# Performance work log

Measured on AMD Instinct MI355X. Metric: run time of the kernel, lower is better.

The kernel has to match this reference:

```python
import jax, jax.numpy as jnp
import numpy as np

COS_EPS = 1e-08


def setup_inputs() -> dict:
    key = jax.random.key(0)
    k1, k2, k3, k4, k5 = jax.random.split(key, 5)
    B, N, C = 4, 4096, 128
    q_node = jax.random.normal(k1, (B, N, C), dtype=jnp.float32)
    k_node = jax.random.normal(k2, (B, N, C), dtype=jnp.float32)
    v_node = jax.random.normal(k3, (B, N, C), dtype=jnp.float32)
    # shared Linear(h_dim, h_dim): torch default init scale ~ 1/sqrt(C)
    W = jax.random.normal(k4, (C, C), dtype=jnp.float32) / jnp.sqrt(jnp.float32(C))
    b = jax.random.normal(k5, (C,), dtype=jnp.float32) / jnp.sqrt(jnp.float32(C))
    return {"q_node": q_node, "k_node": k_node, "v_node": v_node, "W": W, "b": b}


def reference(q_node, k_node, v_node, W, b):
    # shared projection applied to q, k, v
    q = jnp.einsum('bnc,cd->bnd', q_node, W.T) + b
    k = jnp.einsum('bnc,cd->bnd', k_node, W.T) + b
    v = jnp.einsum('bnc,cd->bnd', v_node, W.T) + b
    # cosine similarity scores: [B, Nq, Nk]
    qn = jnp.linalg.norm(q, axis=2, keepdims=True)        # [B, Nq, 1]
    kn = jnp.linalg.norm(k, axis=2, keepdims=True)        # [B, Nk, 1]
    scores = jnp.einsum('bqc,bkc->bqk', q, k)
    cos_sim = scores / (qn * jnp.swapaxes(kn, 1, 2) + COS_EPS)
    # sum-normalization (not softmax)
    edge_weight = cos_sim / (cos_sim.sum(axis=2, keepdims=True) + 1e-08)
    # weighted aggregation: [B, Nq, C]
    return jnp.einsum('bqk,bkc->bqc', edge_weight, v)
```

## Files before the change

kernel.cpp:

```cpp
#include <hip/hip_runtime.h>

#define BB 4
#define NN 4096
#define CC 128
#define NROWS (BB * NN)

#define QN_OFF  0
#define QP_OFF  (QN_OFF + NROWS)
#define MM_OFF  (QP_OFF + NROWS * CC)
#define KS_OFF  (MM_OFF + BB * CC * CC)
#define PP_OFF  (KS_OFF + BB * CC)
#define KP_OFF  (PP_OFF + 256 * CC * CC)

__device__ __forceinline__ void fma4(float4& a, const float4 x,
    const float4 w0, const float4 w1, const float4 w2, const float4 w3)
{
    a.x += x.x * w0.x + x.y * w1.x + x.z * w2.x + x.w * w3.x;
    a.y += x.x * w0.y + x.y * w1.y + x.z * w2.y + x.w * w3.y;
    a.z += x.x * w0.z + x.y * w1.z + x.z * w2.z + x.w * w3.z;
    a.w += x.x * w0.w + x.y * w1.w + x.z * w2.w + x.w * w3.w;
}

__device__ __forceinline__ float dot4(const float4 x, const float4 k)
{
    return x.x * k.x + x.y * k.y + x.z * k.z + x.w * k.w;
}

__global__ __launch_bounds__(512, 2) void projpb_kernel(
    const float* __restrict__ q_node, const float* __restrict__ k_node,
    const float* __restrict__ v_node, const float* __restrict__ W,
    const float* __restrict__ bias, float* __restrict__ ws)
{
    __shared__ float S[CC * CC];
    __shared__ float4 red[512];
    const int tid = threadIdx.x;

    for (int e = tid; e < CC * CC; e += 512) {
        int d = e >> 7, c = e & 127;
        S[(c << 7) + ((((d >> 2) ^ (c & 31)) << 2) | (d & 3))] = W[e];
    }

    const int blk  = blockIdx.x;
    const int base = blk * 64;
    const int dg = tid & 31;
    const int rg = tid >> 5;

    float4 bias4 = ((const float4*)bias)[dg];
    float4 acc[8];
#pragma unroll
    for (int i = 0; i < 8; i++) acc[i] = bias4;

    __syncthreads();

    const float4* Qv = (const float4*)(q_node + (size_t)(base + rg * 4) * CC);
    const float4* Kv = (const float4*)(k_node + (size_t)(base + rg * 4) * CC);
    const float4* Sv = (const float4*)S;

#define LW(s0, s1, s2, s3, c)                              \
    s0 = Sv[(((c) + 0) << 5) + (dg ^ (((c) + 0) & 31))];   \
    s1 = Sv[(((c) + 1) << 5) + (dg ^ (((c) + 1) & 31))];   \
    s2 = Sv[(((c) + 2) << 5) + (dg ^ (((c) + 2) & 31))];   \
    s3 = Sv[(((c) + 3) << 5) + (dg ^ (((c) + 3) & 31))];
#define LX(xq, xk, c)                                      \
    { const int c4_ = (c) >> 2;                            \
      xq[0] = Qv[c4_];      xq[1] = Qv[32 + c4_];          \
      xq[2] = Qv[64 + c4_]; xq[3] = Qv[96 + c4_];          \
      xk[0] = Kv[c4_];      xk[1] = Kv[32 + c4_];          \
      xk[2] = Kv[64 + c4_]; xk[3] = Kv[96 + c4_]; }
#define FM(w0, w1, w2, w3, xq, xk)                         \
    fma4(acc[0], xq[0], w0, w1, w2, w3);                   \
    fma4(acc[1], xq[1], w0, w1, w2, w3);                   \
    fma4(acc[2], xq[2], w0, w1, w2, w3);                   \
    fma4(acc[3], xq[3], w0, w1, w2, w3);                   \
    fma4(acc[4], xk[0], w0, w1, w2, w3);                   \
    fma4(acc[5], xk[1], w0, w1, w2, w3);                   \
    fma4(acc[6], xk[2], w0, w1, w2, w3);                   \
    fma4(acc[7], xk[3], w0, w1, w2, w3);

    {
        float4 wA0, wA1, wA2, wA3, wB0, wB1, wB2, wB3;
        float4 xqA[4], xkA[4], xqB[4], xkB[4];

        LW(wA0, wA1, wA2, wA3, 0)
        LX(xqA, xkA, 0)
        for (int c = 0; c <= CC - 16; c += 8) {
            LW(wB0, wB1, wB2, wB3, c + 4)
            LX(xqB, xkB, c + 4)
            FM(wA0, wA1, wA2, wA3, xqA, xkA)
            LW(wA0, wA1, wA2, wA3, c + 8)
            LX(xqA, xkA, c + 8)
            FM(wB0, wB1, wB2, wB3, xqB, xkB)
        }
        LW(wB0, wB1, wB2, wB3, CC - 4)
        LX(xqB, xkB, CC - 4)
        FM(wA0, wA1, wA2, wA3, xqA, xkA)
        FM(wB0, wB1, wB2, wB3, xqB, xkB)
    }
#undef LW
#undef LX
#undef FM

#pragma unroll
    for (int i = 0; i < 4; i++) {
        const int rq = base + rg * 4 + i;
        float ss = acc[i].x * acc[i].x + acc[i].y * acc[i].y
                 + acc[i].z * acc[i].z + acc[i].w * acc[i].w;
#pragma unroll
        for (int off = 16; off > 0; off >>= 1) ss += __shfl_xor(ss, off, 32);
        ((float4*)(ws + QP_OFF + (size_t)rq * CC))[dg] = acc[i];
        if (dg == 0) ws[QN_OFF + rq] = sqrtf(ss);
    }

    __syncthreads();

    float* Khs = S;
    float* Vs  = S + 8192;

#pragma unroll
    for (int i = 0; i < 4; i++) {
        float ss = acc[4 + i].x * acc[4 + i].x + acc[4 + i].y * acc[4 + i].y
                 + acc[4 + i].z * acc[4 + i].z + acc[4 + i].w * acc[4 + i].w;
#pragma unroll
        for (int off = 16; off > 0; off >>= 1) ss += __shfl_xor(ss, off, 32);
        float inv = 1.0f / sqrtf(ss);
        float4 o = acc[4 + i];
        o.x *= inv; o.y *= inv; o.z *= inv; o.w *= inv;
        ((float4*)(Khs + (rg * 4 + i) * CC))[dg] = o;
    }

    const int c4v = tid & 31, nrv = tid >> 5;
    const float* Vp = v_node + (size_t)base * CC;
#pragma unroll
    for (int i = 0; i < 4; i++) {
        int n = nrv + i * 16;
        ((float4*)(Vs + n * CC))[c4v] = ((const float4*)(Vp + (size_t)n * CC))[c4v];
    }
    __syncthreads();

    float4 ksum4 = make_float4(0.f, 0.f, 0.f, 0.f);
#pragma unroll
    for (int i = 0; i < 4; i++) {
        int n = nrv + i * 16;
        float4 kv = ((const float4*)(Khs + n * CC))[c4v];
        ksum4.x += kv.x; ksum4.y += kv.y; ksum4.z += kv.z; ksum4.w += kv.w;
    }

    const int dg2 = tid & 15, cg = tid >> 4;
    float a2[4][8];
#pragma unroll
    for (int i = 0; i < 4; i++)
#pragma unroll
        for (int j = 0; j < 8; j++) a2[i][j] = 0.f;

#define P2L(ka, va, vb, n)                                  \
    ka = *(const float4*)(Khs + (n) * CC + 4 * cg);         \
    va = *(const float4*)(Vs + (n) * CC + 4 * dg2);         \
    vb = *(const float4*)(Vs + (n) * CC + 64 + 4 * dg2);
#define P2F(ka, va, vb)                                     \
    {  float kc[4] = {ka.x, ka.y, ka.z, ka.w};              \
       float vd[8] = {va.x, va.y, va.z, va.w,               \
                      vb.x, vb.y, vb.z, vb.w};              \
       _Pragma("unroll")                                    \
       for (int i = 0; i < 4; i++)                          \
           { _Pragma("unroll")                              \
             for (int j = 0; j < 8; j++)                    \
                 a2[i][j] += kc[i] * vd[j]; } }

    {
        float4 kaA, vaA, vbA, kaB, vaB, vbB;
        P2L(kaA, vaA, vbA, 0)
        for (int n = 0; n <= 60; n += 2) {
            P2L(kaB, vaB, vbB, n + 1)
            P2F(kaA, vaA, vbA)
            P2L(kaA, vaA, vbA, n + 2)
            P2F(kaB, vaB, vbB)
        }
        P2L(kaB, vaB, vbB, 63)
        P2F(kaA, vaA, vbA)
        P2F(kaB, vaB, vbB)
    }
#undef P2L
#undef P2F

    float* pp = ws + PP_OFF + (size_t)blk * (CC * CC);
#pragma unroll
    for (int i = 0; i < 4; i++) {
        int c = 4 * cg + i;
        *(float4*)(pp + c * CC + 4 * dg2) =
            make_float4(a2[i][0], a2[i][1], a2[i][2], a2[i][3]);
        *(float4*)(pp + c * CC + 64 + 4 * dg2) =
            make_float4(a2[i][4], a2[i][5], a2[i][6], a2[i][7]);
    }

    red[nrv * 32 + c4v] = ksum4;
    __syncthreads();
    if (tid < 32) {
        float4 sm = red[tid];
#pragma unroll
        for (int i = 1; i < 16; i++) {
            float4 t = red[i * 32 + tid];
            sm.x += t.x; sm.y += t.y; sm.z += t.z; sm.w += t.w;
        }
        ((float4*)(ws + KP_OFF + (size_t)blk * CC))[tid] = sm;
    }
}

__global__ __launch_bounds__(256) void mchain_kernel(const float* __restrict__ W,
                                                     const float* __restrict__ bias,
                                                     float* __restrict__ ws)
{
    __shared__ float4 W4s[CC * 32];
    __shared__ float4 m0q[4][2][32];
    __shared__ float m0row[2][CC];
    __shared__ float kpart[4];
    __shared__ float ksl[2];
    const int tid = threadIdx.x;
    const int b = blockIdx.y, x = blockIdx.x;
    const int c0 = x * 2;

    for (int idx = tid; idx < CC * 32; idx += 256) {
        int e = idx >> 5, d4 = idx & 31;
        W4s[(e << 5) + (d4 ^ (e & 31))] = ((const float4*)W)[idx];
    }

    {
        const int q  = tid >> 6;
        const int r  = (tid >> 5) & 1;
        const int c4 = tid & 31;
        const float4* pp = (const float4*)(ws + PP_OFF
                         + (size_t)(b * 64 + q * 16) * (CC * CC)
                         + (size_t)(c0 + r) * CC) + c4;
        float4 s0 = make_float4(0.f, 0.f, 0.f, 0.f);
#pragma unroll 4
        for (int p = 0; p < 16; p++) {
            float4 t = pp[(size_t)p * (CC * CC / 4)];
            s0.x += t.x; s0.y += t.y; s0.z += t.z; s0.w += t.w;
        }
        m0q[q][r][c4] = s0;
    }

    {
        const int rr = tid >> 7, p = tid & 127;
        float v = 0.f;
        if (p < 64) v = ws[KP_OFF + (size_t)(b * 64 + p) * CC + c0 + rr];
#pragma unroll
        for (int off = 32; off > 0; off >>= 1) v += __shfl_xor(v, off, 64);
        if ((tid & 63) == 0) kpart[tid >> 6] = v;
    }
    __syncthreads();

    if (tid < 64) {
        const int r = tid >> 5, c4 = tid & 31;
        float4 a = m0q[0][r][c4], bq = m0q[1][r][c4];
        float4 c = m0q[2][r][c4], d = m0q[3][r][c4];
        float4 s;
        s.x = (a.x + bq.x) + (c.x + d.x);
        s.y = (a.y + bq.y) + (c.y + d.y);
        s.z = (a.z + bq.z) + (c.z + d.z);
        s.w = (a.w + bq.w) + (c.w + d.w);
        ((float4*)&m0row[r][0])[c4] = s;
    }
    if (tid < 2) {
        float s = kpart[tid * 2] + kpart[tid * 2 + 1];
        ksl[tid] = s;
        ws[KS_OFF + b * CC + c0 + tid] = s;
    }
    __syncthreads();

    const int r = tid >> 7, e = tid & 127;
    const float4* mr = (const float4*)m0row[r];
    float m = 0.f;
#pragma unroll
    for (int d4 = 0; d4 < 32; d4++) {
        float4 a4 = mr[d4];
        float4 w4 = W4s[(e << 5) + (d4 ^ (e & 31))];
        m += a4.x * w4.x + a4.y * w4.y + a4.z * w4.z + a4.w * w4.w;
    }
    m += ksl[r] * bias[e];
    ws[MM_OFF + (size_t)b * CC * CC + (size_t)(c0 + r) * CC + e] = m;
}

__global__ __launch_bounds__(512, 2) void out_kernel(const float* __restrict__ ws,
                                                     float* __restrict__ out)
{
    __shared__ float Ml[CC * CC];

    const int blk = blockIdx.x;
    const int b = blk >> 6;
    const int r0 = (blk & 63) * 64;
    const float* M = ws + MM_OFF + (size_t)b * CC * CC;
    const int tid = threadIdx.x;

    for (int e = tid; e < CC * CC / 4; e += 512)
        ((float4*)Ml)[e] = ((const float4*)M)[e];

    const float4* Ks4 = (const float4*)(ws + KS_OFF + b * CC);
    const int dg = tid & 31, rg = tid >> 5;
    const int row = r0 + rg * 4;
    const float4* Qv = (const float4*)(ws + QP_OFF + ((size_t)b * NN + row) * CC);
    const float4* Mv = (const float4*)Ml;

    float4 acc[4];
    float s[4];
#pragma unroll
    for (int i = 0; i < 4; i++) {
        acc[i] = make_float4(0.f, 0.f, 0.f, 0.f);
        s[i] = 0.f;
    }

    __syncthreads();

#define OLW(m0, m1, m2, m3, ks, c)               \
    m0 = Mv[(((c) + 0) << 5) + dg];              \
    m1 = Mv[(((c) + 1) << 5) + dg];              \
    m2 = Mv[(((c) + 2) << 5) + dg];              \
    m3 = Mv[(((c) + 3) << 5) + dg];              \
    ks = Ks4[(c) >> 2];
#define OLX(xv, c)                                 \
    { const int c4_ = (c) >> 2;                    \
      xv[0] = Qv[c4_];      xv[1] = Qv[32 + c4_];  \
      xv[2] = Qv[64 + c4_]; xv[3] = Qv[96 + c4_]; }
#define OFM(m0, m1, m2, m3, ks, xv)                  \
    _Pragma("unroll")                                \
    for (int i_ = 0; i_ < 4; i_++) {                 \
        fma4(acc[i_], xv[i_], m0, m1, m2, m3);       \
        s[i_] += dot4(xv[i_], ks);                   \
    }

    {
        float4 mA0, mA1, mA2, mA3, mB0, mB1, mB2, mB3;
        float4 ksA, ksB, xA[4], xB[4];
        OLW(mA0, mA1, mA2, mA3, ksA, 0)
        OLX(xA, 0)
        for (int c = 0; c <= CC - 16; c += 8) {
            OLW(mB0, mB1, mB2, mB3, ksB, c + 4)
            OLX(xB, c + 4)
            OFM(mA0, mA1, mA2, mA3, ksA, xA)
            OLW(mA0, mA1, mA2, mA3, ksA, c + 8)
            OLX(xA, c + 8)
            OFM(mB0, mB1, mB2, mB3, ksB, xB)
        }
        OLW(mB0, mB1, mB2, mB3, ksB, CC - 4)
        OLX(xB, CC - 4)
        OFM(mA0, mA1, mA2, mA3, ksA, xA)
        OFM(mB0, mB1, mB2, mB3, ksB, xB)
    }
#undef OLW
#undef OLX
#undef OFM

    float* op = out + ((size_t)b * NN + row) * CC;
    const float* qn = ws + QN_OFF + (size_t)b * NN + row;
#pragma unroll
    for (int i = 0; i < 4; i++) {
        float inv = 1.0f / (s[i] + 1e-8f * qn[i]);
        float4 o = acc[i];
        o.x *= inv; o.y *= inv; o.z *= inv; o.w *= inv;
        ((float4*)(op + (size_t)i * CC))[dg] = o;
    }
}

extern "C" void kernel_launch(void* const* d_in, const int* in_sizes, int n_in,
                              void* d_out, int out_size, void* d_ws, size_t ws_size,
                              hipStream_t stream)
{
    const float* q_node = (const float*)d_in[0];
    const float* k_node = (const float*)d_in[1];
    const float* v_node = (const float*)d_in[2];
    const float* W      = (const float*)d_in[3];
    const float* bias   = (const float*)d_in[4];
    float* out = (float*)d_out;
    float* ws  = (float*)d_ws;

    projpb_kernel<<<256, 512, 0, stream>>>(q_node, k_node, v_node, W, bias, ws);
    mchain_kernel<<<dim3(64, BB), 256, 0, stream>>>(W, bias, ws);
    out_kernel<<<256, 512, 0, stream>>>(ws, out);
}
```

Baseline: 131.6 us.

## Use bf16x3 split MFMA for shared Q/K projection in first kernel

Measured after the change: 121.3 us. 1.09x faster.

```diff
diff --git a/kernel.cpp b/kernel.cpp
--- a/kernel.cpp
+++ b/kernel.cpp
@@ -12,6 +12,9 @@
 #define PP_OFF  (KS_OFF + BB * CC)
 #define KP_OFF  (PP_OFF + 256 * CC * CC)
 
+typedef __attribute__((ext_vector_type(8))) short short8;
+typedef __attribute__((ext_vector_type(4))) float f32x4;
+
 __device__ __forceinline__ void fma4(float4& a, const float4 x,
     const float4 w0, const float4 w1, const float4 w2, const float4 w3)
 {
@@ -26,106 +29,132 @@
     return x.x * k.x + x.y * k.y + x.z * k.z + x.w * k.w;
 }
 
-__global__ __launch_bounds__(512, 2) void projpb_kernel(
+__device__ __forceinline__ unsigned short f2bf(float f)
+{
+    union { float f; unsigned u; } v; v.f = f;
+    unsigned r = (v.u + 0x7fffu + ((v.u >> 16) & 1u)) >> 16;
+    return (unsigned short)r;
+}
+__device__ __forceinline__ float bf2f(unsigned short h)
+{
+    union { unsigned u; float f; } v; v.u = ((unsigned)h) << 16;
+    return v.f;
+}
+
+__global__ __launch_bounds__(512, 1) void projpb_kernel(
     const float* __restrict__ q_node, const float* __restrict__ k_node,
     const float* __restrict__ v_node, const float* __restrict__ W,
     const float* __restrict__ bias, float* __restrict__ ws)
 {
-    __shared__ float S[CC * CC];
+    __shared__ __align__(16) unsigned short Wsp[3 * CC * CC];
     __shared__ float4 red[512];
+    unsigned short* Whi = Wsp;
+    unsigned short* Wmd = Wsp + CC * CC;
+    unsigned short* Wlo = Wsp + 2 * CC * CC;
+
     const int tid = threadIdx.x;
 
     for (int e = tid; e < CC * CC; e += 512) {
-        int d = e >> 7, c = e & 127;
-        S[(c << 7) + ((((d >> 2) ^ (c & 31)) << 2) | (d & 3))] = W[e];
+        int col = e >> 7, k = e & 127;
+        float wv = W[e];
+        unsigned short hi = f2bf(wv);
+        float r1 = wv - bf2f(hi);
+        unsigned short md = f2bf(r1);
+        unsigned short lo = f2bf(r1 - bf2f(md));
+        int idx = (col << 7) + ((((k >> 3) ^ (col & 7)) << 3) | (k & 7));
+        Whi[idx] = hi; Wmd[idx] = md; Wlo[idx] = lo;
     }
 
     const int blk  = blockIdx.x;
     const int base = blk * 64;
-    const int dg = tid & 31;
-    const int rg = tid >> 5;
-
-    float4 bias4 = ((const float4*)bias)[dg];
-    float4 acc[8];
-#pragma unroll
-    for (int i = 0; i < 8; i++) acc[i] = bias4;
-
-    __syncthreads();
-
-    const float4* Qv = (const float4*)(q_node + (size_t)(base + rg * 4) * CC);
-    const float4* Kv = (const float4*)(k_node + (size_t)(base + rg * 4) * CC);
-    const float4* Sv = (const float4*)S;
-
-#define LW(s0, s1, s2, s3, c)                              \
-    s0 = Sv[(((c) + 0) << 5) + (dg ^ (((c) + 0) & 31))];   \
-    s1 = Sv[(((c) + 1) << 5) + (dg ^ (((c) + 1) & 31))];   \
-    s2 = Sv[(((c) + 2) << 5) + (dg ^ (((c) + 2) & 31))];   \
-    s3 = Sv[(((c) + 3) << 5) + (dg ^ (((c) + 3) & 31))];
-#define LX(xq, xk, c)                                      \
-    { const int c4_ = (c) >> 2;                            \
-      xq[0] = Qv[c4_];      xq[1] = Qv[32 + c4_];          \
-      xq[2] = Qv[64 + c4_]; xq[3] = Qv[96 + c4_];          \
-      xk[0] = Kv[c4_];      xk[1] = Kv[32 + c4_];          \
-      xk[2] = Kv[64 + c4_]; xk[3] = Kv[96 + c4_]; }
-#define FM(w0, w1, w2, w3, xq, xk)                         \
-    fma4(acc[0], xq[0], w0, w1, w2, w3);                   \
-    fma4(acc[1], xq[1], w0, w1, w2, w3);                   \
-    fma4(acc[2], xq[2], w0, w1, w2, w3);                   \
-    fma4(acc[3], xq[3], w0, w1, w2, w3);                   \
-    fma4(acc[4], xk[0], w0, w1, w2, w3);                   \
-    fma4(acc[5], xk[1], w0, w1, w2, w3);                   \
-    fma4(acc[6], xk[2], w0, w1, w2, w3);                   \
-    fma4(acc[7], xk[3], w0, w1, w2, w3);
-
-    {
-        float4 wA0, wA1, wA2, wA3, wB0, wB1, wB2, wB3;
-        float4 xqA[4], xkA[4], xqB[4], xkB[4];
-
-        LW(wA0, wA1, wA2, wA3, 0)
-        LX(xqA, xkA, 0)
-        for (int c = 0; c <= CC - 16; c += 8) {
-            LW(wB0, wB1, wB2, wB3, c + 4)
-            LX(xqB, xkB, c + 4)
-            FM(wA0, wA1, wA2, wA3, xqA, xkA)
-            LW(wA0, wA1, wA2, wA3, c + 8)
-            LX(xqA, xkA, c + 8)
-            FM(wB0, wB1, wB2, wB3, xqB, xkB)
-        }
-        LW(wB0, wB1, wB2, wB3, CC - 4)
-        LX(xqB, xkB, CC - 4)
-        FM(wA0, wA1, wA2, wA3, xqA, xkA)
-        FM(wB0, wB1, wB2, wB3, xqB, xkB)
-    }
-#undef LW
-#undef LX
-#undef FM
-
-#pragma unroll
-    for (int i = 0; i < 4; i++) {
-        const int rq = base + rg * 4 + i;
-        float ss = acc[i].x * acc[i].x + acc[i].y * acc[i].y
-                 + acc[i].z * acc[i].z + acc[i].w * acc[i].w;
-#pragma unroll
-        for (int off = 16; off > 0; off >>= 1) ss += __shfl_xor(ss, off, 32);
-        ((float4*)(ws + QP_OFF + (size_t)rq * CC))[dg] = acc[i];
-        if (dg == 0) ws[QN_OFF + rq] = sqrtf(ss);
-    }
-
-    __syncthreads();
-
-    float* Khs = S;
-    float* Vs  = S + 8192;
-
-#pragma unroll
-    for (int i = 0; i < 4; i++) {
-        float ss = acc[4 + i].x * acc[4 + i].x + acc[4 + i].y * acc[4 + i].y
-                 + acc[4 + i].z * acc[4 + i].z + acc[4 + i].w * acc[4 + i].w;
-#pragma unroll
-        for (int off = 16; off > 0; off >>= 1) ss += __shfl_xor(ss, off, 32);
-        float inv = 1.0f / sqrtf(ss);
-        float4 o = acc[4 + i];
-        o.x *= inv; o.y *= inv; o.z *= inv; o.w *= inv;
-        ((float4*)(Khs + (rg * 4 + i) * CC))[dg] = o;
+    const int w    = tid >> 6;
+    const int lane = tid & 63;
+    const int l15  = lane & 15;
+    const int lg   = lane >> 4;
+    const bool isq = (w < 4);
+    const int rt   = w & 3;
+    const float* X = isq ? q_node : k_node;
+    const int arow = base + rt * 16 + l15;
+
+    f32x4 acc[8];
+#pragma unroll
+    for (int ct = 0; ct < 8; ct++) {
+        float b = bias[ct * 16 + l15];
+        acc[ct] = (f32x4){b, b, b, b};
+    }
+
+    __syncthreads();
+
+    const float* Xr = X + (size_t)arow * CC;
+#pragma unroll
+    for (int ks = 0; ks < 4; ks++) {
+        const int k0 = ks * 32 + lg * 8;
+        float4 xa = *(const float4*)(Xr + k0);
+        float4 xb = *(const float4*)(Xr + k0 + 4);
+        float xs[8] = {xa.x, xa.y, xa.z, xa.w, xb.x, xb.y, xb.z, xb.w};
+        short8 Ahi, Amd, Alo;
+#pragma unroll
+        for (int j = 0; j < 8; j++) {
+            unsigned short h = f2bf(xs[j]);
+            float r1 = xs[j] - bf2f(h);
+            unsigned short m = f2bf(r1);
+            Ahi[j] = (short)h;
+            Amd[j] = (short)m;
+            Alo[j] = (short)f2bf(r1 - bf2f(m));
+        }
+        const int slot = ks * 4 + lg;
+#pragma unroll
+        for (int ct = 0; ct < 8; ct++) {
+            int col  = ct * 16 + l15;
+            int fidx = (col << 7) + ((slot ^ (col & 7)) << 3);
+            short8 Bhi = *(const short8*)(Whi + fidx);
+            short8 Bmd = *(const short8*)(Wmd + fidx);
+            short8 Blo = *(const short8*)(Wlo + fidx);
+            acc[ct] = __builtin_amdgcn_mfma_f32_16x16x32_bf16(Ahi, Bhi, acc[ct], 0, 0, 0);
+            acc[ct] = __builtin_amdgcn_mfma_f32_16x16x32_bf16(Ahi, Bmd, acc[ct], 0, 0, 0);
+            acc[ct] = __builtin_amdgcn_mfma_f32_16x16x32_bf16(Amd, Bhi, acc[ct], 0, 0, 0);
+            acc[ct] = __builtin_amdgcn_mfma_f32_16x16x32_bf16(Ahi, Blo, acc[ct], 0, 0, 0);
+            acc[ct] = __builtin_amdgcn_mfma_f32_16x16x32_bf16(Amd, Bmd, acc[ct], 0, 0, 0);
+            acc[ct] = __builtin_amdgcn_mfma_f32_16x16x32_bf16(Alo, Bhi, acc[ct], 0, 0, 0);
+        }
+    }
+
+    float ss[4];
+#pragma unroll
+    for (int r = 0; r < 4; r++) {
+        float t = 0.f;
+#pragma unroll
+        for (int ct = 0; ct < 8; ct++) t += acc[ct][r] * acc[ct][r];
+#pragma unroll
+        for (int off = 8; off > 0; off >>= 1) t += __shfl_xor(t, off, 16);
+        ss[r] = t;
+    }
+
+    if (isq) {
+#pragma unroll
+        for (int r = 0; r < 4; r++) {
+            int gr = base + rt * 16 + lg * 4 + r;
+            float* qp = ws + QP_OFF + (size_t)gr * CC;
+#pragma unroll
+            for (int ct = 0; ct < 8; ct++) qp[ct * 16 + l15] = acc[ct][r];
+            if (l15 == 0) ws[QN_OFF + gr] = sqrtf(ss[r]);
+        }
+    }
+
+    __syncthreads();
+
+    float* Khs = (float*)Wsp;
+    float* Vs  = Khs + 8192;
+
+    if (!isq) {
+#pragma unroll
+        for (int r = 0; r < 4; r++) {
+            float inv = 1.0f / sqrtf(ss[r]);
+            int lr = rt * 16 + lg * 4 + r;
+            float* kp = Khs + lr * CC;
+#pragma unroll
+            for (int ct = 0; ct < 8; ct++) kp[ct * 16 + l15] = acc[ct][r] * inv;
+        }
     }
 
     const int c4v = tid & 31, nrv = tid >> 5;
```
